# Performance work log

Measured on AMD Instinct MI355X. Metric: run time of the kernel, lower is better.

## Reference

```python
import jax, jax.numpy as jnp
import numpy as np

B, CIN, H, W = 8, 256, 128, 128
DIM, K, NCLS = 32, 2048, 20
M, T = 0.999, 0.4
N_SEL = B * H * W // 2  # sal masks have exactly half foreground


def _l2norm(x, axis):
    n = jnp.sqrt(jnp.sum(x * x, axis=axis, keepdims=True))
    return x / jnp.maximum(n, 1e-12)


def _balanced_bce(logits, labels):
    # BalancedCrossEntropyLoss (astmt-style), size_average=True
    labels = (labels >= 0.5).astype(logits.dtype)
    n_pos = jnp.sum(labels)
    n_neg = labels.size - n_pos
    gz = (logits >= 0).astype(logits.dtype)
    # stable log-sigmoid formulation
    loss_val = logits * (labels - gz) - jnp.log1p(jnp.exp(logits - 2.0 * logits * gz))
    loss_pos = jnp.sum(-labels * loss_val)
    loss_neg = jnp.sum(-(1.0 - labels) * loss_val)
    tot = n_pos + n_neg
    return (n_neg / tot * loss_pos + n_pos / tot * loss_neg) / labels.size


def setup_inputs() -> dict:
    key = jax.random.key(0)
    ks = jax.random.split(key, 8)
    im_q = jax.random.normal(ks[0], (B, CIN, H, W), dtype=jnp.float32)
    im_k = jax.random.normal(ks[1], (B, CIN, H, W), dtype=jnp.float32)
    # checkerboard saliency: exactly half the pixels are foreground
    sal = (jnp.arange(B * H * W, dtype=jnp.int32) % 2).reshape(B, H, W)
    W_q = jax.random.normal(ks[2], (DIM, CIN), dtype=jnp.float32) * 0.05
    W_bg = jax.random.normal(ks[3], (1, CIN), dtype=jnp.float32) * 0.05
    W_k = jax.random.normal(ks[4], (DIM, CIN), dtype=jnp.float32) * 0.05
    W_cls = jax.random.normal(ks[5], (NCLS, DIM), dtype=jnp.float32) * 0.05
    q0 = jax.random.normal(ks[6], (DIM, K), dtype=jnp.float32)
    obj_queue = _l2norm(q0, 0)
    return {"im_q": im_q, "sal_q": sal, "im_k": im_k, "sal_k": sal,
            "W_q": W_q, "W_bg": W_bg, "W_k": W_k, "W_cls": W_cls,
            "obj_queue": obj_queue}


def reference(im_q, sal_q, im_k, sal_k, W_q, W_bg, W_k, W_cls, obj_queue):
    # --- query encoder (1x1-conv feature head + bg head) ---
    q = jnp.einsum('oc,bchw->bohw', W_q, im_q)          # [B, DIM, H, W]
    q = _l2norm(q, 1)
    q_bg = jnp.einsum('oc,bchw->bohw', W_bg, im_q)[:, 0]  # [B, H, W]
    sal_loss = _balanced_bce(q_bg, sal_q.astype(q.dtype))

    # --- classifier (1x1 conv) ---
    cluster = jnp.einsum('oc,bchw->bhwo', W_cls, q).reshape(-1, NCLS)

    # --- pixel -> image-index labeling via saliency mask ---
    offset = jnp.arange(0, 2 * B, 2, dtype=sal_q.dtype)
    lab = ((sal_q + offset[:, None, None]) * sal_q).reshape(-1)
    mask_indexes = jnp.nonzero(lab, size=N_SEL, fill_value=0)[0]
    sal_sel = lab[mask_indexes] // 2                     # [N_SEL] image index per fg pixel

    # --- momentum key encoder + object prototypes (no grad) ---
    W_k_m = M * W_k + (1.0 - M) * W_q
    k = jnp.einsum('oc,bchw->bohw', W_k_m, im_k)
    k = _l2norm(k, 1).reshape(B, DIM, H * W)
    salk = sal_k.reshape(B, H * W).astype(k.dtype)
    protos = _l2norm(jnp.einsum('bdn,bn->bd', k, salk), 1)  # [B, DIM]

    # --- gather foreground pixels ---
    q_flat = q.transpose(0, 2, 3, 1).reshape(-1, DIM)
    q_sel = q_flat[mask_indexes]                          # [N_SEL, DIM]
    cl_sel = cluster[mask_indexes]
    # opt == 2: keep only per-pixel max cluster logit, pseudo labels are zeros
    cl_sel = jnp.max(cl_sel, axis=1, keepdims=True)       # [N_SEL, 1]
    pseudo_labels = jnp.zeros((N_SEL,), dtype=jnp.int32)

    # --- contrastive logits: drop own prototype column per row ---
    batch_logits = q_sel @ protos.T                       # [N_SEL, B]
    cols = jnp.arange(B - 1)
    take = cols[None, :] + (cols[None, :] >= sal_sel[:, None]).astype(cols.dtype)
    batch_logits = jnp.take_along_axis(batch_logits, take, axis=1)  # [N_SEL, B-1]

    bank_logits = q_sel @ obj_queue                       # [N_SEL, K]
    logits = jnp.concatenate([cl_sel, batch_logits, bank_logits], axis=1) / T

    # --- dequeue-and-enqueue (ptr = 0) ---
    new_queue = jax.lax.dynamic_update_slice(obj_queue, protos.T, (0, 0))
    return logits, pseudo_labels, sal_loss, new_queue
```

## Files before the change

kernel.cpp:

```cpp
#include <hip/hip_runtime.h>

typedef __attribute__((ext_vector_type(8))) short short8;
typedef __attribute__((ext_vector_type(4))) float f32x4;
typedef __attribute__((ext_vector_type(2))) float f32x2;

constexpr int CIN  = 256;
constexpr int HWp  = 16384;
constexpr int NSEL = 65536;
constexpr int NCOLS = 2056;

constexpr size_t OUT_PL   = (size_t)NSEL * NCOLS;
constexpr size_t OUT_LOSS = OUT_PL + NSEL;
constexpr size_t OUT_NQ   = OUT_LOSS + 1;

constexpr size_t WS_TILECNT  = 0;
constexpr size_t WS_TILEBASE = 2048;
constexpr size_t WS_NPOS     = 4096;
constexpr size_t WS_LPLN     = 4104;
constexpr size_t WS_WQT      = 8192;
constexpr size_t WS_WKMT     = 40960;
constexpr size_t WS_PSUM     = 73728;
constexpr size_t WS_PROTO    = 74752;
constexpr size_t WS_QT       = 131072;
constexpr size_t WS_CLSEL    = 262144;
constexpr size_t WS_SALSEL   = 524288;
constexpr size_t WS_QSEL     = 1048576;

static __device__ __forceinline__ unsigned short f2bf(float f) {
  const unsigned x = __float_as_uint(f);
  return (unsigned short)((x + 0x7fffu + ((x >> 16) & 1u)) >> 16);
}
static __device__ __forceinline__ float bf2f(unsigned short u) {
  return __uint_as_float(((unsigned)u) << 16);
}

__global__ __launch_bounds__(256) void kP1(const int* __restrict__ salq, int* __restrict__ tileCnt,
                                           const float* __restrict__ Wq, const float* __restrict__ Wk,
                                           float* __restrict__ wqt, float* __restrict__ wkmt,
                                           float* __restrict__ psum, float* __restrict__ lpln) {
  const int g = blockIdx.x, t = threadIdx.x;
  __shared__ int red[256];
  const int base = g << 9;
  red[t] = ((salq[base + 2 * t] != 0) ? 1 : 0) + ((salq[base + 2 * t + 1] != 0) ? 1 : 0);
  __syncthreads();
  for (int s = 128; s > 0; s >>= 1) { if (t < s) red[t] += red[t + s]; __syncthreads(); }
  if (t == 0) tileCnt[g] = red[0];
  if (g < 32) {
    const int idx = (g << 8) + t;
    const int o = idx & 31, c = idx >> 5;
    const float wq = Wq[o * 256 + c];
    wqt[idx] = wq;
    wkmt[idx] = 0.999f * Wk[o * 256 + c] + 0.001f * wq;
  }
  if (g == 32) { psum[t] = 0.f; if (t < 2) lpln[t] = 0.f; }
}

__global__ __launch_bounds__(256) void kP2(const int* __restrict__ tileCnt, int* __restrict__ tileBase,
                                           int* __restrict__ nposp) {
  const int t = threadIdx.x;
  __shared__ int sc[256];
  const int c0 = tileCnt[t];
  sc[t] = c0;
  __syncthreads();
  for (int off = 1; off < 256; off <<= 1) {
    int v = (t >= off) ? sc[t - off] : 0;
    __syncthreads();
    sc[t] += v;
    __syncthreads();
  }
  tileBase[t] = sc[t] - c0;
  if (t == 255) *nposp = sc[255];
}

__global__ __launch_bounds__(256) void kAB(
    const float* __restrict__ imq, const float* __restrict__ imk,
    const int* __restrict__ salq, const int* __restrict__ salk,
    const float* __restrict__ wqt, const float* __restrict__ wkmt,
    const float* __restrict__ wbg, const float* __restrict__ wcls,
    const int* __restrict__ tileBase,
    ushort* __restrict__ qsel, float* __restrict__ clsel, int* __restrict__ salsel,
    float* __restrict__ lpln, float* __restrict__ psum) {
  const int g = blockIdx.x, t = threadIdx.x;
  const bool isA = (g < 256);
  const int tile = isA ? g : (g - 256);
  const int base = tile << 9;
  const int b = base >> 14;
  const int n = (base & (HWp - 1)) + (t << 1);
  const float* __restrict__ ip = (isA ? imq : imk) + (size_t)b * (CIN * HWp) + n;
  const float* __restrict__ wt0 = isA ? wqt : wkmt;

  float a0[32], a1[32];
#pragma unroll
  for (int o = 0; o < 32; ++o) { a0[o] = 0.f; a1[o] = 0.f; }
  float bg0 = 0.f, bg1 = 0.f;

#pragma unroll 8
  for (int c = 0; c < 256; ++c) {
    const f32x2 v = __builtin_nontemporal_load(
        reinterpret_cast<const f32x2*>(ip + (size_t)c * HWp));
    const float* wt = wt0 + (c << 5);
    const float wb = wbg[c];
#pragma unroll
    for (int o = 0; o < 32; ++o) {
      a0[o] = fmaf(wt[o], v.x, a0[o]);
      a1[o] = fmaf(wt[o], v.y, a1[o]);
    }
    bg0 = fmaf(wb, v.x, bg0);
    bg1 = fmaf(wb, v.y, bg1);
  }

  const int lane = t & 63, wv = t >> 6;
  const int flat0 = base + (t << 1);

  if (isA) {
    const int s0 = (salq[flat0] != 0) ? 1 : 0;
    const int s1 = (salq[flat0 + 1] != 0) ? 1 : 0;
    const unsigned spair = (unsigned)(s0 + s1);
    unsigned incl = spair;
#pragma unroll
    for (int off = 1; off < 64; off <<= 1) {
      unsigned u = __shfl_up(incl, off);
      if (lane >= off) incl += u;
    }
    __shared__ int wtot[4];
    if (lane == 63) wtot[wv] = (int)incl;
    __syncthreads();
    int wbase = 0;
    for (int i = 0; i < wv; ++i) wbase += wtot[i];
    const int excl = tileBase[tile] + wbase + (int)(incl - spair);

#pragma unroll
    for (int i = 0; i < 2; ++i) {
      const int si = i ? s1 : s0;
      const int rank = i ? (excl + s0) : excl;
      if (si && rank < NSEL) {
        float ss = 0.f;
#pragma unroll
        for (int o = 0; o < 32; ++o) { const float a = i ? a1[o] : a0[o]; ss = fmaf(a, a, ss); }
        const float inv = 1.f / fmaxf(sqrtf(ss), 1e-12f);
        float qn[32];
#pragma unroll
        for (int o = 0; o < 32; ++o) qn[o] = (i ? a1[o] : a0[o]) * inv;
        float m = -3.402823466e38f;
#pragma unroll
        for (int j = 0; j < 20; ++j) {
          float d = 0.f;
#pragma unroll
          for (int o = 0; o < 32; ++o) d = fmaf(wcls[(j << 5) + o], qn[o], d);
          m = fmaxf(m, d);
        }
        clsel[rank] = m;
        salsel[rank] = b;
        ushort* qp = qsel + ((size_t)rank << 5);
#pragma unroll
        for (int v4 = 0; v4 < 4; ++v4) {
          short8 v8;
#pragma unroll
          for (int j = 0; j < 8; ++j) v8[j] = (short)f2bf(qn[(v4 << 3) + j]);
          *reinterpret_cast<short8*>(qp + (v4 << 3)) = v8;
        }
      }
    }
    const float gz0 = (bg0 >= 0.f) ? 1.f : 0.f;
    const float gz1 = (bg1 >= 0.f) ? 1.f : 0.f;
    const float lv0 = bg0 * ((float)s0 - gz0) - log1pf(expf(bg0 - 2.f * bg0 * gz0));
    const float lv1 = bg1 * ((float)s1 - gz1) - log1pf(expf(bg1 - 2.f * bg1 * gz1));
    float lp = -(s0 ? lv0 : 0.f) - (s1 ? lv1 : 0.f);
    float ln = -(s0 ? 0.f : lv0) - (s1 ? 0.f : lv1);
#pragma unroll
    for (int off = 32; off > 0; off >>= 1) { lp += __shfl_down(lp, off); ln += __shfl_down(ln, off); }
    __shared__ float slp[4], sln[4];
    if (lane == 0) { slp[wv] = lp; sln[wv] = ln; }
    __syncthreads();
    if (t == 0) {
      atomicAdd(&lpln[0], slp[0] + slp[1] + slp[2] + slp[3]);
      atomicAdd(&lpln[1], sln[0] + sln[1] + sln[2] + sln[3]);
    }
  } else {
    const int s0 = (salk[flat0] != 0) ? 1 : 0;
    const int s1 = (salk[flat0 + 1] != 0) ? 1 : 0;
    float ss0 = 0.f, ss1 = 0.f;
#pragma unroll
    for (int o = 0; o < 32; ++o) { ss0 = fmaf(a0[o], a0[o], ss0); ss1 = fmaf(a1[o], a1[o], ss1); }
    const float inv0 = s0 ? (1.f / fmaxf(sqrtf(ss0), 1e-12f)) : 0.f;
    const float inv1 = s1 ? (1.f / fmaxf(sqrtf(ss1), 1e-12f)) : 0.f;
    float p[32];
#pragma unroll
    for (int o = 0; o < 32; ++o) p[o] = a0[o] * inv0 + a1[o] * inv1;
#pragma unroll
    for (int o = 0; o < 32; ++o) {
#pragma unroll
      for (int off = 32; off > 0; off >>= 1) p[o] += __shfl_down(p[o], off);
    }
    __shared__ float sp[4][32];
    if (lane == 0) {
#pragma unroll
      for (int o = 0; o < 32; ++o) sp[wv][o] = p[o];
    }
    __syncthreads();
    if (t < 32) atomicAdd(&psum[(b << 5) + t], sp[0][t] + sp[1][t] + sp[2][t] + sp[3][t]);
  }
}

__global__ __launch_bounds__(256) void kC(const float* __restrict__ objq, const float* __restrict__ psum,
                                          const float* __restrict__ lpln, const int* __restrict__ nposp,
                                          float* __restrict__ proto, ushort* __restrict__ qt,
                                          float* __restrict__ nq, float* __restrict__ outLoss) {
  const int g = blockIdx.x, t = threadIdx.x;
  if (g == 256) {
    __shared__ float sq[256];
    __shared__ float sinv[8];
    const float v = psum[t];
    sq[t] = v * v;
    __syncthreads();
    if (t < 8) {
      float s = 0.f;
      for (int o = 0; o < 32; ++o) s += sq[(t << 5) + o];
      sinv[t] = 1.f / fmaxf(sqrtf(s), 1e-12f);
    }
    __syncthreads();
    const float pv = v * sinv[t >> 5];
    proto[t] = pv;
    const int p = t >> 5, o = t & 31;
    nq[(size_t)o * 2048 + p] = pv;
    if (t == 0) {
      const float np = (float)(*nposp);
      outLoss[0] = ((131072.f - np) / 131072.f * lpln[0] + np / 131072.f * lpln[1]) / 131072.f;
    }
  } else {
    const int idx = (g << 8) + t;
    const int o = idx >> 11, j = idx & 2047;
    const float v = objq[idx];
    qt[(j << 5) + o] = f2bf(v);
    if (j >= 8) nq[idx] = v;
  }
}

__global__ __launch_bounds__(256) void kDE(const ushort* __restrict__ qsel, const ushort* __restrict__ qt,
                                           const float* __restrict__ proto, const float* __restrict__ clsel,
                                           const int* __restrict__ salsel,
                                           float* __restrict__ out, int* __restrict__ pl) {
  __shared__ float buf[16][1028];
  __shared__ float dd[16][9];
  __shared__ float hd[16][8];
  const int t = threadIdx.x, g = blockIdx.x;
  const int wv = t >> 6, lane = t & 63;
  const int r0 = g << 4;
  if (t < 16) pl[r0 + t] = 0;

  const int rlo = lane & 15, kh = lane >> 4;
  const f32x4 zero = {0.f, 0.f, 0.f, 0.f};

  const short8 bfrag = *reinterpret_cast<const short8*>(
      qsel + (size_t)(r0 + rlo) * 32 + kh * 8);
  const ushort* qa = qt + rlo * 32 + kh * 8;
  float* obase = out + (size_t)r0 * NCOLS;

  if (t < 128) {
    const int ri = t >> 3, pp = t & 7;
    const short8* qp = reinterpret_cast<const short8*>(qsel + ((size_t)(r0 + ri) << 5));
    float s = 0.f;
#pragma unroll
    for (int i = 0; i < 4; ++i) {
      const short8 v8 = qp[i];
#pragma unroll
      for (int j = 0; j < 8; ++j)
        s = fmaf(proto[(pp << 5) + (i << 3) + j], bf2f((unsigned short)v8[j]), s);
    }
    dd[ri][pp] = s;
  }
  __syncthreads();

  if (t < 16) {
    const int b = salsel[r0 + t];
    hd[t][0] = clsel[r0 + t] * 2.5f;
#pragma unroll
    for (int c = 0; c < 7; ++c) {
      const int pi = c + ((c >= b) ? 1 : 0);
      hd[t][1 + c] = dd[t][pi] * 2.5f;
    }
  }
#pragma unroll 8
  for (int ct2 = 0; ct2 < 16; ++ct2) {
    const int lt = (wv << 4) + ct2;
    const short8 afrag = *reinterpret_cast<const short8*>(qa + (size_t)lt * 512);
    f32x4 r = __builtin_amdgcn_mfma_f32_16x16x32_bf16(afrag, bfrag, zero, 0, 0, 0);
    r *= 2.5f;
    *reinterpret_cast<f32x4*>(&buf[rlo][(lt << 4) + (kh << 2)]) = r;
  }
  __syncthreads();
  if (t < 32) {
    const int rr = t >> 1, cc = (t & 1) << 2;
    *reinterpret_cast<f32x4*>(obase + (size_t)rr * NCOLS + cc) =
        *reinterpret_cast<const f32x4*>(&hd[rr][cc]);
  }
#pragma unroll
  for (int rr = 0; rr < 16; ++rr) {
    const f32x4 v = *reinterpret_cast<const f32x4*>(&buf[rr][t << 2]);
    *reinterpret_cast<f32x4*>(obase + (size_t)rr * NCOLS + 8 + (t << 2)) = v;
  }
  __syncthreads();

#pragma unroll 8
  for (int ct2 = 0; ct2 < 16; ++ct2) {
    const int lt = (wv << 4) + ct2;
    const short8 afrag = *reinterpret_cast<const short8*>(qa + (size_t)(lt + 64) * 512);
    f32x4 r = __builtin_amdgcn_mfma_f32_16x16x32_bf16(afrag, bfrag, zero, 0, 0, 0);
    r *= 2.5f;
    *reinterpret_cast<f32x4*>(&buf[rlo][(lt << 4) + (kh << 2)]) = r;
  }
  __syncthreads();
#pragma unroll
  for (int rr = 0; rr < 16; ++rr) {
    const f32x4 v = *reinterpret_cast<const f32x4*>(&buf[rr][t << 2]);
    *reinterpret_cast<f32x4*>(obase + (size_t)rr * NCOLS + 1032 + (t << 2)) = v;
  }
}

extern "C" void kernel_launch(void* const* d_in, const int* in_sizes, int n_in,
                              void* d_out, int out_size, void* d_ws, size_t ws_size,
                              hipStream_t stream) {
  const float* imq  = (const float*)d_in[0];
  const int*   salq = (const int*)d_in[1];
  const float* imk  = (const float*)d_in[2];
  const int*   salk = (const int*)d_in[3];
  const float* Wq   = (const float*)d_in[4];
  const float* Wbg  = (const float*)d_in[5];
  const float* Wk   = (const float*)d_in[6];
  const float* Wcls = (const float*)d_in[7];
  const float* objq = (const float*)d_in[8];
  float* out = (float*)d_out;
  char* ws = (char*)d_ws;

  int*    tileCnt  = (int*)(ws + WS_TILECNT);
  int*    tileBase = (int*)(ws + WS_TILEBASE);
  int*    nposp    = (int*)(ws + WS_NPOS);
  float*  lpln     = (float*)(ws + WS_LPLN);
  float*  wqt      = (float*)(ws + WS_WQT);
  float*  wkmt     = (float*)(ws + WS_WKMT);
  float*  psum     = (float*)(ws + WS_PSUM);
  float*  proto    = (float*)(ws + WS_PROTO);
  ushort* qt       = (ushort*)(ws + WS_QT);
  float*  clsel    = (float*)(ws + WS_CLSEL);
  int*    salsel   = (int*)(ws + WS_SALSEL);
  ushort* qsel     = (ushort*)(ws + WS_QSEL);

  hipLaunchKernelGGL(kP1, dim3(256), dim3(256), 0, stream, salq, tileCnt, Wq, Wk, wqt, wkmt, psum, lpln);
  hipLaunchKernelGGL(kP2, dim3(1), dim3(256), 0, stream, tileCnt, tileBase, nposp);
  hipLaunchKernelGGL(kAB, dim3(512), dim3(256), 0, stream, imq, imk, salq, salk, wqt, wkmt,
                     Wbg, Wcls, tileBase, qsel, clsel, salsel, lpln, psum);
  hipLaunchKernelGGL(kC, dim3(257), dim3(256), 0, stream, objq, psum, lpln, nposp, proto, qt,
                     out + OUT_NQ, out + OUT_LOSS);
  hipLaunchKernelGGL(kDE, dim3(4096), dim3(256), 0, stream, qsel, qt, proto, clsel, salsel,
                     out, (int*)(out + OUT_PL));
}
```

Baseline: 242.0 us.

## Double-buffer kDE output staging to overlap MFMA compute with global stores

The bank-logit section of kDE used to fill one large 16x1024 shared buffer per half and then store it. It now works in eight 256-column chunks, ping-ponging between two small shared buffers so that storing chunk c-1 overlaps with the MFMA compute for chunk c. This cuts shared memory from about 64KB to about 33KB per block, which may allow more resident blocks, at the cost of more __syncthreads barriers.

```diff
diff --git a/kernel.cpp b/kernel.cpp
--- a/kernel.cpp
+++ b/kernel.cpp
@@ -240,7 +240,7 @@
                                            const float* __restrict__ proto, const float* __restrict__ clsel,
                                            const int* __restrict__ salsel,
                                            float* __restrict__ out, int* __restrict__ pl) {
-  __shared__ float buf[16][1028];
+  __shared__ float buf[2][16][260];
   __shared__ float dd[16][9];
   __shared__ float hd[16][8];
   const int t = threadIdx.x, g = blockIdx.x;
@@ -270,7 +270,6 @@
     dd[ri][pp] = s;
   }
   __syncthreads();
-
   if (t < 16) {
     const int b = salsel[r0 + t];
     hd[t][0] = clsel[r0 + t] * 2.5f;
@@ -280,40 +279,48 @@
       hd[t][1 + c] = dd[t][pi] * 2.5f;
     }
   }
-#pragma unroll 8
-  for (int ct2 = 0; ct2 < 16; ++ct2) {
-    const int lt = (wv << 4) + ct2;
-    const short8 afrag = *reinterpret_cast<const short8*>(qa + (size_t)lt * 512);
-    f32x4 r = __builtin_amdgcn_mfma_f32_16x16x32_bf16(afrag, bfrag, zero, 0, 0, 0);
+
+  short8 af[4];
+#pragma unroll
+  for (int i = 0; i < 4; ++i)
+    af[i] = *reinterpret_cast<const short8*>(qa + (size_t)((wv << 2) + i) * 512);
+#pragma unroll
+  for (int i = 0; i < 4; ++i) {
+    f32x4 r = __builtin_amdgcn_mfma_f32_16x16x32_bf16(af[i], bfrag, zero, 0, 0, 0);
     r *= 2.5f;
-    *reinterpret_cast<f32x4*>(&buf[rlo][(lt << 4) + (kh << 2)]) = r;
+    *reinterpret_cast<f32x4*>(&buf[0][rlo][(((wv << 2) + i) << 4) + (kh << 2)]) = r;
   }
   __syncthreads();
-  if (t < 32) {
-    const int rr = t >> 1, cc = (t & 1) << 2;
-    *reinterpret_cast<f32x4*>(obase + (size_t)rr * NCOLS + cc) =
-        *reinterpret_cast<const f32x4*>(&hd[rr][cc]);
-  }
-#pragma unroll
-  for (int rr = 0; rr < 16; ++rr) {
-    const f32x4 v = *reinterpret_cast<const f32x4*>(&buf[rr][t << 2]);
-    *reinterpret_cast<f32x4*>(obase + (size_t)rr * NCOLS + 8 + (t << 2)) = v;
-  }
-  __syncthreads();
-
-#pragma unroll 8
-  for (int ct2 = 0; ct2 < 16; ++ct2) {
-    const int lt = (wv << 4) + ct2;
-    const short8 afrag = *reinterpret_cast<const short8*>(qa + (size_t)(lt + 64) * 512);
-    f32x4 r = __builtin_amdgcn_mfma_f32_16x16x32_bf16(afrag, bfrag, zero, 0, 0, 0);
-    r *= 2.5f;
-    *reinterpret_cast<f32x4*>(&buf[rlo][(lt << 4) + (kh << 2)]) = r;
-  }
-  __syncthreads();
-#pragma unroll
-  for (int rr = 0; rr < 16; ++rr) {
-    const f32x4 v = *reinterpret_cast<const f32x4*>(&buf[rr][t << 2]);
-    *reinterpret_cast<f32x4*>(obase + (size_t)rr * NCOLS + 1032 + (t << 2)) = v;
+
+  for (int c = 1; c < 8; ++c) {
+    const int pb = (c - 1) & 1, cb = c & 1;
+#pragma unroll
+    for (int i = 0; i < 4; ++i)
+      af[i] = *reinterpret_cast<const short8*>(qa + (size_t)((c << 4) + (wv << 2) + i) * 512);
+    if (c == 1 && t < 32) {
+      const int rr = t >> 1, cc = (t & 1) << 2;
+      *reinterpret_cast<f32x4*>(obase + (size_t)rr * NCOLS + cc) =
+          *reinterpret_cast<const f32x4*>(&hd[rr][cc]);
+    }
+#pragma unroll
+    for (int it = 0; it < 4; ++it) {
+      const int row = (it << 2) + wv;
+      const f32x4 v = *reinterpret_cast<const f32x4*>(&buf[pb][row][lane << 2]);
+      *reinterpret_cast<f32x4*>(obase + (size_t)row * NCOLS + 8 + ((c - 1) << 8) + (lane << 2)) = v;
+    }
+#pragma unroll
+    for (int i = 0; i < 4; ++i) {
+      f32x4 r = __builtin_amdgcn_mfma_f32_16x16x32_bf16(af[i], bfrag, zero, 0, 0, 0);
+      r *= 2.5f;
+      *reinterpret_cast<f32x4*>(&buf[cb][rlo][(((wv << 2) + i) << 4) + (kh << 2)]) = r;
+    }
+    __syncthreads();
+  }
+#pragma unroll
+  for (int it = 0; it < 4; ++it) {
+    const int row = (it << 2) + wv;
+    const f32x4 v = *reinterpret_cast<const f32x4*>(&buf[1][row][lane << 2]);
+    *reinterpret_cast<f32x4*>(obase + (size_t)row * NCOLS + 8 + (7 << 8) + (lane << 2)) = v;
   }
 }
 
```

Result: slower. 257.9 us (+6.6%).
